# Optimization experiments

Measured on AMD Instinct MI355X. Metric: run time of the kernel, lower is better.

Reference implementation:

```python
import jax, jax.numpy as jnp
import numpy as np

B, C, L = 16, 256, 1024
DIM_U, Q_EMB = 64, 64
INTER = DIM_U * Q_EMB  # 4096
EPS = 1e-5

def setup_inputs() -> dict:
    key = jax.random.key(0)
    ks = jax.random.split(key, 7)
    x = jax.random.normal(ks[0], (B, C, L), dtype=jnp.float32)
    u_i = jax.random.normal(ks[1], (B, DIM_U), dtype=jnp.float32)
    e_qid = jax.random.normal(ks[2], (B, Q_EMB, L), dtype=jnp.float32)
    t = jax.random.normal(ks[3], (B, 1, L), dtype=jnp.float32)
    # nn.Linear weights: (out_features, in_features), Kaiming-uniform-ish init
    wb = 1.0 / np.sqrt(INTER)
    W = jax.random.uniform(ks[4], (2 * C, INTER), jnp.float32, -wb, wb)
    V = jax.random.uniform(ks[5], (2 * C, 1), jnp.float32, -1.0, 1.0)
    bias = jnp.zeros((2 * C,), dtype=jnp.float32)
    return {"x": x, "u_i": u_i, "e_qid": e_qid, "t": t, "W": W, "V": V, "bias": bias}

def reference(x, u_i, e_qid, t, W, V, bias):
    # InstanceNorm1d (affine=False): per-(b,c) stats over L, biased variance
    mean = jnp.mean(x, axis=-1, keepdims=True)
    var = jnp.mean(jnp.square(x - mean), axis=-1, keepdims=True)
    nx = (x - mean) * jax.lax.rsqrt(var + EPS)
    # Bilinear conditioning: interaction[b, u*Q+q, l] = u_i[b,u] * e_qid[b,q,l];
    # style = W @ interaction, fused as a single contraction (no BxINTERxL tensor)
    Wr = W.reshape(2 * C, DIM_U, Q_EMB)
    style = jnp.einsum('bu,bql,cuq->bcl', u_i, e_qid, Wr)  # (B, 2C, L)
    time = jnp.einsum('bol,co->bcl', t, V)                  # (B, 2C, L)
    params = style + time + bias[None, :, None]
    gamma, beta = jnp.split(params, 2, axis=1)
    return (1.0 + gamma) * nx + beta
```

## Files before the change

kernel.cpp:

```cpp
#include <hip/hip_runtime.h>

#define NB 16
#define NC 256
#define NL 1024
#define NQ 64
#define NU 64
#define N2C 512
#define NINTER 4096
#define CT 32
#define LT 256

__global__ __launch_bounds__(64) void calc_A_kernel(
    const float* __restrict__ u_i, const float* __restrict__ W,
    float* __restrict__ A) {
  const int c2 = blockIdx.x;
  const int q = threadIdx.x;
  float acc[NB];
#pragma unroll
  for (int b = 0; b < NB; ++b) acc[b] = 0.0f;
  const float* Wrow = W + c2 * NINTER;
#pragma unroll 4
  for (int u = 0; u < NU; ++u) {
    const float w = Wrow[u * NQ + q];
#pragma unroll
    for (int b = 0; b < NB; ++b) acc[b] = fmaf(u_i[b * NU + u], w, acc[b]);
  }
#pragma unroll
  for (int b = 0; b < NB; ++b) A[(b * N2C + c2) * NQ + q] = acc[b];
}

__global__ __launch_bounds__(256) void stats_kernel(
    const float* __restrict__ x, float* __restrict__ mean,
    float* __restrict__ rstd) {
  const int row = blockIdx.x;
  const int t = threadIdx.x;
  const float4 v = reinterpret_cast<const float4*>(x)[row * (NL / 4) + t];
  float s = v.x + v.y + v.z + v.w;
  float ss = v.x * v.x + v.y * v.y + v.z * v.z + v.w * v.w;
#pragma unroll
  for (int off = 32; off >= 1; off >>= 1) {
    s += __shfl_xor(s, off, 64);
    ss += __shfl_xor(ss, off, 64);
  }
  __shared__ float ls[4], lss[4];
  const int w = t >> 6;
  if ((t & 63) == 0) { ls[w] = s; lss[w] = ss; }
  __syncthreads();
  if (t == 0) {
    const float S = ls[0] + ls[1] + ls[2] + ls[3];
    const float SS = lss[0] + lss[1] + lss[2] + lss[3];
    const float m = S * (1.0f / NL);
    const float var = SS * (1.0f / NL) - m * m;
    mean[row] = m;
    rstd[row] = rsqrtf(var + 1e-5f);
  }
}

__global__ __launch_bounds__(256) void fused_kernel(
    const float* __restrict__ x, const float* __restrict__ e,
    const float* __restrict__ tt, const float* __restrict__ V,
    const float* __restrict__ bias, const float* __restrict__ A,
    const float* __restrict__ mean, const float* __restrict__ rstd,
    float* __restrict__ out) {
  __shared__ float eT[32][LT];
  __shared__ float Ag[CT][NQ];
  __shared__ float Ab[CT][NQ];
  __shared__ float sm[CT], sr[CT];

  const int blk = blockIdx.x;
  const int b = blk >> 5;
  const int ct = (blk >> 2) & 7;
  const int lt = blk & 3;
  const int t = threadIdx.x;

  {
    const float4* Asg =
        reinterpret_cast<const float4*>(A + (b * N2C + ct * CT) * NQ);
    const float4* Asb =
        reinterpret_cast<const float4*>(A + (b * N2C + NC + ct * CT) * NQ);
    float4* Agv = reinterpret_cast<float4*>(&Ag[0][0]);
    float4* Abv = reinterpret_cast<float4*>(&Ab[0][0]);
#pragma unroll
    for (int k = 0; k < 2; ++k) {
      Agv[t + k * 256] = Asg[t + k * 256];
      Abv[t + k * 256] = Asb[t + k * 256];
    }
  }
  if (t < CT) {
    sm[t] = mean[b * NC + ct * CT + t];
    sr[t] = rstd[b * NC + ct * CT + t];
  }

  const int w = t >> 6, ln = t & 63;
  float4 g4[8], p4[8];
#pragma unroll
  for (int s = 0; s < 8; ++s) {
    g4[s] = make_float4(0.f, 0.f, 0.f, 0.f);
    p4[s] = make_float4(0.f, 0.f, 0.f, 0.f);
  }

  for (int half = 0; half < 2; ++half) {
    if (half) __syncthreads();
    {
      const float* ebase = e + b * NQ * NL + half * 32 * NL + lt * LT;
#pragma unroll
      for (int k = 0; k < 8; ++k) {
        const int idx = t + k * 256;
        const int q = idx >> 6;
        const int j = idx & 63;
        reinterpret_cast<float4*>(&eT[q][0])[j] =
            reinterpret_cast<const float4*>(ebase + q * NL)[j];
      }
    }
    __syncthreads();

#pragma unroll 2
    for (int q0 = 0; q0 < 32; q0 += 4) {
      const float4 e0 = reinterpret_cast<const float4*>(&eT[q0 + 0][0])[ln];
      const float4 e1 = reinterpret_cast<const float4*>(&eT[q0 + 1][0])[ln];
      const float4 e2 = reinterpret_cast<const float4*>(&eT[q0 + 2][0])[ln];
      const float4 e3 = reinterpret_cast<const float4*>(&eT[q0 + 3][0])[ln];
      const int qa = half * 32 + q0;
#pragma unroll
      for (int s = 0; s < 8; ++s) {
        const int r = w * 8 + s;
        const float4 a = *reinterpret_cast<const float4*>(&Ag[r][qa]);
        g4[s].x = fmaf(a.x, e0.x, fmaf(a.y, e1.x, fmaf(a.z, e2.x, fmaf(a.w, e3.x, g4[s].x))));
        g4[s].y = fmaf(a.x, e0.y, fmaf(a.y, e1.y, fmaf(a.z, e2.y, fmaf(a.w, e3.y, g4[s].y))));
        g4[s].z = fmaf(a.x, e0.z, fmaf(a.y, e1.z, fmaf(a.z, e2.z, fmaf(a.w, e3.z, g4[s].z))));
        g4[s].w = fmaf(a.x, e0.w, fmaf(a.y, e1.w, fmaf(a.z, e2.w, fmaf(a.w, e3.w, g4[s].w))));
        const float4 c = *reinterpret_cast<const float4*>(&Ab[r][qa]);
        p4[s].x = fmaf(c.x, e0.x, fmaf(c.y, e1.x, fmaf(c.z, e2.x, fmaf(c.w, e3.x, p4[s].x))));
        p4[s].y = fmaf(c.x, e0.y, fmaf(c.y, e1.y, fmaf(c.z, e2.y, fmaf(c.w, e3.y, p4[s].y))));
        p4[s].z = fmaf(c.x, e0.z, fmaf(c.y, e1.z, fmaf(c.z, e2.z, fmaf(c.w, e3.z, p4[s].z))));
        p4[s].w = fmaf(c.x, e0.w, fmaf(c.y, e1.w, fmaf(c.z, e2.w, fmaf(c.w, e3.w, p4[s].w))));
      }
    }
  }

  const float4 tv = reinterpret_cast<const float4*>(tt + b * NL + lt * LT)[ln];
#pragma unroll
  for (int s = 0; s < 8; ++s) {
    const int r = w * 8 + s;
    const int c = ct * CT + r;
    const float vg = V[c], vb = V[c + NC];
    const float bg = bias[c], bb = bias[c + NC];
    const float m = sm[r], rs = sr[r];
    const float4 xv =
        reinterpret_cast<const float4*>(x + (b * NC + c) * NL + lt * LT)[ln];
    float4 o;
    {
      const float gx = 1.0f + g4[s].x + fmaf(tv.x, vg, bg);
      const float gy = 1.0f + g4[s].y + fmaf(tv.y, vg, bg);
      const float gz = 1.0f + g4[s].z + fmaf(tv.z, vg, bg);
      const float gw = 1.0f + g4[s].w + fmaf(tv.w, vg, bg);
      o.x = fmaf(gx, (xv.x - m) * rs, p4[s].x + fmaf(tv.x, vb, bb));
      o.y = fmaf(gy, (xv.y - m) * rs, p4[s].y + fmaf(tv.y, vb, bb));
      o.z = fmaf(gz, (xv.z - m) * rs, p4[s].z + fmaf(tv.z, vb, bb));
      o.w = fmaf(gw, (xv.w - m) * rs, p4[s].w + fmaf(tv.w, vb, bb));
    }
    reinterpret_cast<float4*>(out + (b * NC + c) * NL + lt * LT)[ln] = o;
  }
}

extern "C" void kernel_launch(void* const* d_in, const int* in_sizes, int n_in,
                              void* d_out, int out_size, void* d_ws,
                              size_t ws_size, hipStream_t stream) {
  const float* x = (const float*)d_in[0];
  const float* u_i = (const float*)d_in[1];
  const float* e = (const float*)d_in[2];
  const float* tt = (const float*)d_in[3];
  const float* W = (const float*)d_in[4];
  const float* V = (const float*)d_in[5];
  const float* bias = (const float*)d_in[6];
  float* out = (float*)d_out;

  float* A = (float*)d_ws;
  float* mean = A + NB * N2C * NQ;
  float* rstd = mean + NB * NC;

  calc_A_kernel<<<N2C, 64, 0, stream>>>(u_i, W, A);
  stats_kernel<<<NB * NC, 256, 0, stream>>>(x, mean, rstd);
  fused_kernel<<<NB * 32, 256, 0, stream>>>(x, e, tt, V, bias, A, mean, rstd,
                                            out);
}
```

Measured before the change: 112.6 us.

## Split calc_A over u with shared reduction; halve L tile, drop e staging

```diff
diff --git a/kernel.cpp b/kernel.cpp
--- a/kernel.cpp
+++ b/kernel.cpp
@@ -8,25 +8,44 @@
 #define N2C 512
 #define NINTER 4096
 #define CT 32
-#define LT 256
+#define LT 128
 
-__global__ __launch_bounds__(64) void calc_A_kernel(
+__global__ __launch_bounds__(256) void calc_A_kernel(
     const float* __restrict__ u_i, const float* __restrict__ W,
     float* __restrict__ A) {
+  __shared__ float su[NB * NU];
+  __shared__ float part[4][NB][NQ];
+  const int t = threadIdx.x;
   const int c2 = blockIdx.x;
-  const int q = threadIdx.x;
+  const int q = t & 63;
+  const int u4 = t >> 6;
+
+#pragma unroll
+  for (int k = 0; k < 4; ++k) su[t + k * 256] = u_i[t + k * 256];
+  __syncthreads();
+
   float acc[NB];
 #pragma unroll
   for (int b = 0; b < NB; ++b) acc[b] = 0.0f;
-  const float* Wrow = W + c2 * NINTER;
-#pragma unroll 4
-  for (int u = 0; u < NU; ++u) {
-    const float w = Wrow[u * NQ + q];
+
+  const float* Wrow = W + c2 * NINTER + u4 * 16 * NQ;
 #pragma unroll
-    for (int b = 0; b < NB; ++b) acc[b] = fmaf(u_i[b * NU + u], w, acc[b]);
+  for (int uu = 0; uu < 16; ++uu) {
+    const float w = Wrow[uu * NQ + q];
+    const int u = u4 * 16 + uu;
+#pragma unroll
+    for (int b = 0; b < NB; ++b) acc[b] = fmaf(su[b * NU + u], w, acc[b]);
   }
 #pragma unroll
-  for (int b = 0; b < NB; ++b) A[(b * N2C + c2) * NQ + q] = acc[b];
+  for (int b = 0; b < NB; ++b) part[u4][b][q] = acc[b];
+  __syncthreads();
+
+#pragma unroll
+  for (int i = 0; i < 4; ++i) {
+    const int b = (t >> 6) * 4 + i;
+    const float s = part[0][b][q] + part[1][b][q] + part[2][b][q] + part[3][b][q];
+    A[(b * N2C + c2) * NQ + q] = s;
+  }
 }
 
 __global__ __launch_bounds__(256) void stats_kernel(
@@ -56,22 +75,30 @@
   }
 }
 
+__device__ __forceinline__ void fma4(float4& acc, float a, const float4& e) {
+  acc.x = fmaf(a, e.x, acc.x);
+  acc.y = fmaf(a, e.y, acc.y);
+  acc.z = fmaf(a, e.z, acc.z);
+  acc.w = fmaf(a, e.w, acc.w);
+}
+
 __global__ __launch_bounds__(256) void fused_kernel(
     const float* __restrict__ x, const float* __restrict__ e,
     const float* __restrict__ tt, const float* __restrict__ V,
     const float* __restrict__ bias, const float* __restrict__ A,
     const float* __restrict__ mean, const float* __restrict__ rstd,
     float* __restrict__ out) {
-  __shared__ float eT[32][LT];
   __shared__ float Ag[CT][NQ];
   __shared__ float Ab[CT][NQ];
   __shared__ float sm[CT], sr[CT];
 
   const int blk = blockIdx.x;
-  const int b = blk >> 5;
-  const int ct = (blk >> 2) & 7;
-  const int lt = blk & 3;
+  const int b = blk >> 6;
+  const int ct = (blk >> 3) & 7;
+  const int lt = blk & 7;
   const int t = threadIdx.x;
+  const int col = t & 31;
+  const int rg = t >> 5;
 
   {
     const float4* Asg =
@@ -90,76 +117,58 @@
     sm[t] = mean[b * NC + ct * CT + t];
     sr[t] = rstd[b * NC + ct * CT + t];
   }
+  __syncthreads();
 
-  const int w = t >> 6, ln = t & 63;
-  float4 g4[8], p4[8];
+  float4 g[4], p[4];
 #pragma unroll
-  for (int s = 0; s < 8; ++s) {
-    g4[s] = make_float4(0.f, 0.f, 0.f, 0.f);
-    p4[s] = make_float4(0.f, 0.f, 0.f, 0.f);
+  for (int i = 0; i < 4; ++i) {
+    g[i] = make_float4(0.f, 0.f, 0.f, 0.f);
+    p[i] = make_float4(0.f, 0.f, 0.f, 0.f);
   }
 
-  for (int half = 0; half < 2; ++half) {
-    if (half) __syncthreads();
-    {
-      const float* ebase = e + b * NQ * NL + half * 32 * NL + lt * LT;
+  const float* ebase = e + b * NQ * NL + lt * LT;
+#pragma unroll 4
+  for (int q0 = 0; q0 < NQ; q0 += 4) {
+    const float4 e0 = reinterpret_cast<const float4*>(ebase + (q0 + 0) * NL)[col];
+    const float4 e1 = reinterpret_cast<const float4*>(ebase + (q0 + 1) * NL)[col];
+    const float4 e2 = reinterpret_cast<const float4*>(ebase + (q0 + 2) * NL)[col];
+    const float4 e3 = reinterpret_cast<const float4*>(ebase + (q0 + 3) * NL)[col];
 #pragma unroll
-      for (int k = 0; k < 8; ++k) {
-        const int idx = t + k * 256;
-        const int q = idx >> 6;
-        const int j = idx & 63;
-        reinterpret_cast<float4*>(&eT[q][0])[j] =
-            reinterpret_cast<const float4*>(ebase + q * NL)[j];
-      }
-    }
-    __syncthreads();
-
-#pragma unroll 2
-    for (int q0 = 0; q0 < 32; q0 += 4) {
-      const float4 e0 = reinterpret_cast<const float4*>(&eT[q0 + 0][0])[ln];
-      const float4 e1 = reinterpret_cast<const float4*>(&eT[q0 + 1][0])[ln];
-      const float4 e2 = reinterpret_cast<const float4*>(&eT[q0 + 2][0])[ln];
-      const float4 e3 = reinterpret_cast<const float4*>(&eT[q0 + 3][0])[ln];
-      const int qa = half * 32 + q0;
-#pragma unroll
-      for (int s = 0; s < 8; ++s) {
-        const int r = w * 8 + s;
-        const float4 a = *reinterpret_cast<const float4*>(&Ag[r][qa]);
-        g4[s].x = fmaf(a.x, e0.x, fmaf(a.y, e1.x, fmaf(a.z, e2.x, fmaf(a.w, e3.x, g4[s].x))));
-        g4[s].y = fmaf(a.x, e0.y, fmaf(a.y, e1.y, fmaf(a.z, e2.y, fmaf(a.w, e3.y, g4[s].y))));
-        g4[s].z = fmaf(a.x, e0.z, fmaf(a.y, e1.z, fmaf(a.z, e2.z, fmaf(a.w, e3.z, g4[s].z))));
-        g4[s].w = fmaf(a.x, e0.w, fmaf(a.y, e1.w, fmaf(a.z, e2.w, fmaf(a.w, e3.w, g4[s].w))));
-        const float4 c = *reinterpret_cast<const float4*>(&Ab[r][qa]);
-        p4[s].x = fmaf(c.x, e0.x, fmaf(c.y, e1.x, fmaf(c.z, e2.x, fmaf(c.w, e3.x, p4[s].x))));
-        p4[s].y = fmaf(c.x, e0.y, fmaf(c.y, e1.y, fmaf(c.z, e2.y, fmaf(c.w, e3.y, p4[s].y))));
-        p4[s].z = fmaf(c.x, e0.z, fmaf(c.y, e1.z, fmaf(c.z, e2.z, fmaf(c.w, e3.z, p4[s].z))));
-        p4[s].w = fmaf(c.x, e0.w, fmaf(c.y, e1.w, fmaf(c.z, e2.w, fmaf(c.w, e3.w, p4[s].w))));
-      }
+    for (int i = 0; i < 4; ++i) {
+      const int r = rg * 4 + i;
+      const float4 a = *reinterpret_cast<const float4*>(&Ag[r][q0]);
+      fma4(g[i], a.x, e0);
+      fma4(g[i], a.y, e1);
+      fma4(g[i], a.z, e2);
+      fma4(g[i], a.w, e3);
+      const float4 c = *reinterpret_cast<const float4*>(&Ab[r][q0]);
+      fma4(p[i], c.x, e0);
+      fma4(p[i], c.y, e1);
+      fma4(p[i], c.z, e2);
+      fma4(p[i], c.w, e3);
     }
   }
 
-  const float4 tv = reinterpret_cast<const float4*>(tt + b * NL + lt * LT)[ln];
+  const float4 tv = reinterpret_cast<const float4*>(tt + b * NL + lt * LT)[col];
 #pragma unroll
-  for (int s = 0; s < 8; ++s) {
-    const int r = w * 8 + s;
+  for (int i = 0; i < 4; ++i) {
+    const int r = rg * 4 + i;
     const int c = ct * CT + r;
     const float vg = V[c], vb = V[c + NC];
     const float bg = bias[c], bb = bias[c + NC];
     const float m = sm[r], rs = sr[r];
     const float4 xv =
-        reinterpret_cast<const float4*>(x + (b * NC + c) * NL + lt * LT)[ln];
+        reinterpret_cast<const float4*>(x + (b * NC + c) * NL + lt * LT)[col];
     float4 o;
-    {
-      const float gx = 1.0f + g4[s].x + fmaf(tv.x, vg, bg);
-      const float gy = 1.0f + g4[s].y + fmaf(tv.y, vg, bg);
-      const float gz = 1.0f + g4[s].z + fmaf(tv.z, vg, bg);
-      const float gw = 1.0f + g4[s].w + fmaf(tv.w, vg, bg);
-      o.x = fmaf(gx, (xv.x - m) * rs, p4[s].x + fmaf(tv.x, vb, bb));
-      o.y = fmaf(gy, (xv.y - m) * rs, p4[s].y + fmaf(tv.y, vb, bb));
-      o.z = fmaf(gz, (xv.z - m) * rs, p4[s].z + fmaf(tv.z, vb, bb));
-      o.w = fmaf(gw, (xv.w - m) * rs, p4[s].w + fmaf(tv.w, vb, bb));
-    }
-    reinterpret_cast<float4*>(out + (b * NC + c) * NL + lt * LT)[ln] = o;
+    const float gx = 1.0f + g[i].x + fmaf(tv.x, vg, bg);
+    const float gy = 1.0f + g[i].y + fmaf(tv.y, vg, bg);
+    const float gz = 1.0f + g[i].z + fmaf(tv.z, vg, bg);
+    const float gw = 1.0f + g[i].w + fmaf(tv.w, vg, bg);
+    o.x = fmaf(gx, (xv.x - m) * rs, p[i].x + fmaf(tv.x, vb, bb));
+    o.y = fmaf(gy, (xv.y - m) * rs, p[i].y + fmaf(tv.y, vb, bb));
+    o.z = fmaf(gz, (xv.z - m) * rs, p[i].z + fmaf(tv.z, vb, bb));
+    o.w = fmaf(gw, (xv.w - m) * rs, p[i].w + fmaf(tv.w, vb, bb));
+    reinterpret_cast<float4*>(out + (b * NC + c) * NL + lt * LT)[col] = o;
   }
 }
 
@@ -179,8 +188,8 @@
   float* mean = A + NB * N2C * NQ;
   float* rstd = mean + NB * NC;
 
-  calc_A_kernel<<<N2C, 64, 0, stream>>>(u_i, W, A);
+  calc_A_kernel<<<N2C, 256, 0, stream>>>(u_i, W, A);
   stats_kernel<<<NB * NC, 256, 0, stream>>>(x, mean, rstd);
-  fused_kernel<<<NB * 32, 256, 0, stream>>>(x, e, tt, V, bias, A, mean, rstd,
+  fused_kernel<<<NB * 64, 256, 0, stream>>>(x, e, tt, V, bias, A, mean, rstd,
                                             out);
 }
```

After: 108.5 us. 1.04x faster.
